# Optimization experiments

Measured on AMD Instinct MI355X. Metric: run time of the kernel, lower is better.

The kernel has to match this reference:

```python
import jax, jax.numpy as jnp
import numpy as np
from jax import lax

C = 128; G = 8; K = 3; P = K * K; GC = C // G
N, H, W = 4, 96, 96
EPS = 1e-5

def conv_bn_silu(x, w, gamma, beta, rmean, rvar, stride, pad):
    # Conv2d(bias=False) + BatchNorm2d(eval) + SiLU, NCHW
    y = lax.conv_general_dilated(x, w, (stride, stride), [(pad, pad), (pad, pad)],
                                 dimension_numbers=('NCHW', 'OIHW', 'NCHW'))
    s = gamma / jnp.sqrt(rvar + EPS)
    y = y * s[None, :, None, None] + (beta - rmean * s)[None, :, None, None]
    return y * jax.nn.sigmoid(y)

def dcnv3(x, dw_w, dw_b, ln_g, ln_b, off_w, off_b, m_w, m_b, ip_w, ip_b, op_w, op_b):
    # InternImage DCNv3, channels-last input (N,H,W,C), k=3 s=1 pad=1 dil=1 group=G, offset_scale=1
    n, h, w, c = x.shape
    xp = x @ ip_w.T + ip_b  # input_proj
    # offset/mask branch: depthwise 3x3 conv + LayerNorm + GELU on the ORIGINAL input
    dw = lax.conv_general_dilated(x, dw_w, (1, 1), [(1, 1), (1, 1)],
                                  dimension_numbers=('NHWC', 'HWIO', 'NHWC'),
                                  feature_group_count=c) + dw_b
    dw = (dw - dw.mean(-1, keepdims=True)) / jnp.sqrt(dw.var(-1, keepdims=True) + EPS) * ln_g + ln_b
    dw = jax.nn.gelu(dw)
    off = (dw @ off_w.T + off_b).reshape(n, h, w, G, P, 2)  # (..., (dx, dy))
    m = jax.nn.softmax((dw @ m_w.T + m_b).reshape(n, h, w, G, P), -1)
    pad = 1
    hp, wp = h + 2 * pad, w + 2 * pad
    xpad = jnp.pad(xp, ((0, 0), (pad, pad), (pad, pad), (0, 0))).reshape(n, hp, wp, G, GC)
    ky, kx = jnp.meshgrid(jnp.arange(-1, 2, dtype=x.dtype), jnp.arange(-1, 2, dtype=x.dtype), indexing='ij')
    # absolute sampling coords in padded image (grid_sample align_corners=False equivalent)
    py = (jnp.arange(h, dtype=x.dtype) + pad)[None, :, None, None, None] + ky.reshape(-1) + off[..., 1]
    px = (jnp.arange(w, dtype=x.dtype) + pad)[None, None, :, None, None] + kx.reshape(-1) + off[..., 0]
    yf = jnp.floor(py); xf = jnp.floor(px)
    wy = py - yf; wx = px - xf
    y0 = yf.astype(jnp.int32); x0 = xf.astype(jnp.int32)
    n_idx = jnp.arange(n)[:, None, None, None, None]
    g_idx = jnp.arange(G)[None, None, None, :, None]

    def gat(yi, xi):
        valid = ((yi >= 0) & (yi < hp) & (xi >= 0) & (xi < wp)).astype(x.dtype)
        v = xpad[n_idx, jnp.clip(yi, 0, hp - 1), jnp.clip(xi, 0, wp - 1), g_idx]  # (n,h,w,G,P,GC)
        return v * valid[..., None]

    v = (gat(y0, x0) * ((1 - wy) * (1 - wx))[..., None]
         + gat(y0, x0 + 1) * ((1 - wy) * wx)[..., None]
         + gat(y0 + 1, x0) * (wy * (1 - wx))[..., None]
         + gat(y0 + 1, x0 + 1) * (wy * wx)[..., None])
    out = jnp.einsum('nhwgpc,nhwgp->nhwgc', v, m).reshape(n, h, w, c)
    return out @ op_w.T + op_b  # output_proj

def _forward(x0, x1, x2, conv_w, conv_g, conv_b, conv_rm, conv_rv,
             conv1_w, conv1_g, conv1_b, conv1_rm, conv1_rv,
             conv2_w, conv2_g, conv2_b, conv2_rm, conv2_rv,
             dw_w, dw_b, ln_g, ln_b, off_w, off_b, m_w, m_b, ip_w, ip_b, op_w, op_b):
    n, _, h, w = x0.shape
    # x1: 256 ch > 128 -> self.conv (1x1); smaller spatial -> bilinear upsample to HW
    y1 = conv_bn_silu(x1, conv_w, conv_g, conv_b, conv_rm, conv_rv, 1, 0)
    feat_up1 = jax.image.resize(y1, (n, C, h, w), method='bilinear')
    # x2: 64 ch < 128 -> self.conv1 (1x1); larger spatial -> self.conv2 (3x3 s2) to HW
    y2 = conv_bn_silu(x2, conv1_w, conv1_g, conv1_b, conv1_rm, conv1_rv, 1, 0)
    feat_up2 = conv_bn_silu(y2, conv2_w, conv2_g, conv2_b, conv2_rm, conv2_rv, 2, 1)
    d1 = dcnv3(feat_up1.transpose(0, 2, 3, 1), dw_w, dw_b, ln_g, ln_b, off_w, off_b, m_w, m_b, ip_w, ip_b, op_w, op_b)
    d2 = dcnv3(feat_up2.transpose(0, 2, 3, 1), dw_w, dw_b, ln_g, ln_b, off_w, off_b, m_w, m_b, ip_w, ip_b, op_w, op_b)
    a1 = jax.nn.relu(d1).transpose(0, 3, 1, 2)
    a2 = jax.nn.relu(d2).transpose(0, 3, 1, 2)
    return jnp.concatenate([a1, x0, a2], axis=1)  # (N, 3C, H, W)

def setup_inputs():
    ks = jax.random.split(jax.random.key(0), 24)
    f = jnp.float32
    return {
        'x0': jax.random.normal(ks[0], (N, C, H, W), f),
        'x1': jax.random.normal(ks[1], (N, 2 * C, H // 2, W // 2), f),
        'x2': jax.random.normal(ks[2], (N, C // 2, 2 * H, 2 * W), f),
        'conv_w': jax.random.normal(ks[3], (C, 2 * C, 1, 1), f) * 0.05,
        'conv_g': jnp.ones((C,), f), 'conv_b': jnp.zeros((C,), f),
        'conv_rm': jax.random.normal(ks[4], (C,), f) * 0.1,
        'conv_rv': jax.random.uniform(ks[5], (C,), f) + 0.5,
        'conv1_w': jax.random.normal(ks[6], (C, C // 2, 1, 1), f) * 0.08,
        'conv1_g': jnp.ones((C,), f), 'conv1_b': jnp.zeros((C,), f),
        'conv1_rm': jax.random.normal(ks[7], (C,), f) * 0.1,
        'conv1_rv': jax.random.uniform(ks[8], (C,), f) + 0.5,
        'conv2_w': jax.random.normal(ks[9], (C, C, 3, 3), f) * 0.03,
        'conv2_g': jnp.ones((C,), f), 'conv2_b': jnp.zeros((C,), f),
        'conv2_rm': jax.random.normal(ks[10], (C,), f) * 0.1,
        'conv2_rv': jax.random.uniform(ks[11], (C,), f) + 0.5,
        'dw_w': jax.random.normal(ks[12], (3, 3, 1, C), f) * 0.1,
        'dw_b': jnp.zeros((C,), f),
        'ln_g': jnp.ones((C,), f), 'ln_b': jnp.zeros((C,), f),
        'off_w': jax.random.normal(ks[13], (G * P * 2, C), f) * 0.01,
        'off_b': jnp.zeros((G * P * 2,), f),
        'm_w': jax.random.normal(ks[14], (G * P, C), f) * 0.05,
        'm_b': jnp.zeros((G * P,), f),
        'ip_w': jax.random.normal(ks[15], (C, C), f) * 0.05,
        'ip_b': jnp.zeros((C,), f),
        'op_w': jax.random.normal(ks[16], (C, C), f) * 0.05,
        'op_b': jnp.zeros((C,), f),
    }

def reference(x0, x1, x2, conv_w, conv_g, conv_b, conv_rm, conv_rv,
              conv1_w, conv1_g, conv1_b, conv1_rm, conv1_rv,
              conv2_w, conv2_g, conv2_b, conv2_rm, conv2_rv,
              dw_w, dw_b, ln_g, ln_b, off_w, off_b, m_w, m_b, ip_w, ip_b, op_w, op_b):
    return _forward(x0, x1, x2, conv_w, conv_g, conv_b, conv_rm, conv_rv,
                    conv1_w, conv1_g, conv1_b, conv1_rm, conv1_rv,
                    conv2_w, conv2_g, conv2_b, conv2_rm, conv2_rv,
                    dw_w, dw_b, ln_g, ln_b, off_w, off_b, m_w, m_b, ip_w, ip_b, op_w, op_b)
```

## Files before the change

### kernel.cpp

```cpp
#include <hip/hip_runtime.h>
#include <cstdint>
#include <cstddef>

#define EPSV 1e-5f
#define NPIX 9216
#define LDA 136
#define LDK 72

typedef __bf16 bf16;
typedef _Float16 f16;
typedef __attribute__((ext_vector_type(8))) __bf16 bf16x8;
typedef __attribute__((ext_vector_type(4))) __bf16 bf16x4;
typedef __attribute__((ext_vector_type(2))) _Float16 f16x2;
typedef __attribute__((ext_vector_type(4))) float  f32x4;

__device__ __forceinline__ float silu_f(float v) { return v / (1.f + __expf(-v)); }

__global__ __launch_bounds__(256) void prep_kernel(
    const float* __restrict__ conv_w, const float* __restrict__ conv_g,
    const float* __restrict__ conv_b, const float* __restrict__ conv_rm, const float* __restrict__ conv_rv,
    const float* __restrict__ conv1_w, const float* __restrict__ conv1_g,
    const float* __restrict__ conv1_b, const float* __restrict__ conv1_rm, const float* __restrict__ conv1_rv,
    const float* __restrict__ conv2_w, const float* __restrict__ conv2_g,
    const float* __restrict__ conv2_bb, const float* __restrict__ conv2_rm, const float* __restrict__ conv2_rv,
    const float* __restrict__ ip_w, const float* __restrict__ op_w,
    const float* __restrict__ off_w, const float* __restrict__ m_w,
    const float* __restrict__ off_b, const float* __restrict__ m_b,
    float* __restrict__ WTSf, bf16* __restrict__ WTSb)
{
  int idx = blockIdx.x * 256 + threadIdx.x;
  if (idx < 608) {
    if (idx < 128) {
      int co = idx;
      float s = conv_g[co] * rsqrtf(conv_rv[co] + EPSV);
      WTSf[idx] = conv_b[co] - conv_rm[co] * s;
    } else if (idx < 256) {
      int co = idx - 128;
      float s = conv1_g[co] * rsqrtf(conv1_rv[co] + EPSV);
      WTSf[idx] = conv1_b[co] - conv1_rm[co] * s;
    } else if (idx < 384) {
      int co = idx - 256;
      float s = conv2_g[co] * rsqrtf(conv2_rv[co] + EPSV);
      WTSf[idx] = conv2_bb[co] - conv2_rm[co] * s;
    } else {
      int col = idx - 384;
      WTSf[idx] = (col < 144) ? off_b[col] : (col < 216 ? m_b[col - 144] : 0.f);
    }
  } else {
    int j = idx - 608;
    if (j < 32768) {
      int co = j >> 8, ci = j & 255;
      float s = conv_g[co] * rsqrtf(conv_rv[co] + EPSV);
      WTSb[j] = (bf16)(conv_w[co * 256 + ci] * s);
    } else if (j < 40960) {
      int r = j - 32768; int co = r >> 6, ci = r & 63;
      float s = conv1_g[co] * rsqrtf(conv1_rv[co] + EPSV);
      WTSb[j] = (bf16)(conv1_w[co * 64 + ci] * s);
    } else if (j < 188416) {
      int r = j - 40960; int kp = r >> 14; int rr = r & 16383;
      int co = rr >> 7, ci = rr & 127;
      float s = conv2_g[co] * rsqrtf(conv2_rv[co] + EPSV);
      WTSb[j] = (bf16)(conv2_w[(co * 128 + ci) * 9 + kp] * s);
    } else if (j < 204800) {
      int r = j - 188416; int co = r >> 7, ci = r & 127;
      WTSb[j] = (bf16)ip_w[co * 128 + ci];
    } else if (j < 233472) {
      int r = j - 204800; int co = r >> 7, ci = r & 127;
      float v = (co < 144) ? off_w[co * 128 + ci] : (co < 216 ? m_w[(co - 144) * 128 + ci] : 0.f);
      WTSb[j] = (bf16)v;
    } else if (j < 249856) {
      int r = j - 233472; int co = r >> 7, ci = r & 127;
      WTSb[j] = (bf16)op_w[co * 128 + ci];
    }
  }
}

__global__ __launch_bounds__(256) void c1x1_mfma_kernel(
    const float* __restrict__ x, const bf16* __restrict__ W,
    const float* __restrict__ bias, int K, int HW, bf16* __restrict__ outb)
{
  __shared__ bf16 As[64 * LDK];
  __shared__ bf16 Bs[128 * LDK];
  int m0 = blockIdx.x << 6;
  int t = threadIdx.x;
  int n = m0 / HW; int hw0 = m0 - n * HW;
  const float* xn = x + (size_t)n * K * HW;
  int wv = t >> 6, lane = t & 63;
  int lrow = lane & 15, q = lane >> 4;
  int n0 = wv * 32;
  f32x4 acc[4][2];
#pragma unroll
  for (int i = 0; i < 4; ++i)
#pragma unroll
    for (int j = 0; j < 2; ++j)
#pragma unroll
      for (int e = 0; e < 4; ++e) acc[i][j][e] = 0.f;

  for (int k0 = 0; k0 < K; k0 += 64) {
    if (k0) __syncthreads();
    for (int i = t; i < 1024; i += 256) {
      int px = i & 63; int ci4 = (i >> 6) << 2;
      bf16x4 p;
#pragma unroll
      for (int j = 0; j < 4; ++j)
        p[j] = (bf16)xn[(size_t)(k0 + ci4 + j) * HW + hw0 + px];
      *(bf16x4*)&As[px * LDK + ci4] = p;
    }
    for (int i = t; i < 1024; i += 256) {
      int co = i >> 3; int k8 = (i & 7) << 3;
      *(bf16x8*)&Bs[co * LDK + k8] = *(const bf16x8*)&W[(size_t)co * K + k0 + k8];
    }
    __syncthreads();
#pragma unroll
    for (int ks = 0; ks < 2; ++ks) {
      int ko = ks * 32 + q * 8;
      bf16x8 bfr0 = *(const bf16x8*)&Bs[(n0 + lrow) * LDK + ko];
      bf16x8 bfr1 = *(const bf16x8*)&Bs[(n0 + 16 + lrow) * LDK + ko];
#pragma unroll
      for (int mi = 0; mi < 4; ++mi) {
        bf16x8 afr = *(const bf16x8*)&As[(mi * 16 + lrow) * LDK + ko];
        acc[mi][0] = __builtin_amdgcn_mfma_f32_16x16x32_bf16(afr, bfr0, acc[mi][0], 0, 0, 0);
        acc[mi][1] = __builtin_amdgcn_mfma_f32_16x16x32_bf16(afr, bfr1, acc[mi][1], 0, 0, 0);
      }
    }
  }
#pragma unroll
  for (int mi = 0; mi < 4; ++mi) {
#pragma unroll
    for (int nj = 0; nj < 2; ++nj) {
      int co = n0 + nj * 16 + lrow;
      float bb = bias[co];
#pragma unroll
      for (int r = 0; r < 4; ++r) {
        int m = m0 + mi * 16 + q * 4 + r;
        outb[(size_t)m * 128 + co] = (bf16)silu_f(acc[mi][nj][r] + bb);
      }
    }
  }
}

__global__ __launch_bounds__(256) void upsample_kernel(
    const bf16* __restrict__ y1b, bf16* __restrict__ feat1b)
{
  int idx = blockIdx.x * 256 + threadIdx.x;
  int c4 = (idx & 31) << 2;
  int pw = idx >> 5;
  int ow = pw % 96; int t1 = pw / 96;
  int oh = t1 % 96; int n = t1 / 96;
  float sh = oh * 0.5f - 0.25f, sw = ow * 0.5f - 0.25f;
  float hf = floorf(sh), wf = floorf(sw);
  float fy = sh - hf, fx = sw - wf;
  int h0 = (int)hf, w0 = (int)wf;
  int h0c = max(h0, 0), h1c = min(h0 + 1, 47);
  int w0c = max(w0, 0), w1c = min(w0 + 1, 47);
  const bf16* yn = y1b + (size_t)n * 2304 * 128 + c4;
  bf16x4 v00 = *(const bf16x4*)&yn[(h0c * 48 + w0c) * 128];
  bf16x4 v01 = *(const bf16x4*)&yn[(h0c * 48 + w1c) * 128];
  bf16x4 v10 = *(const bf16x4*)&yn[(h1c * 48 + w0c) * 128];
  bf16x4 v11 = *(const bf16x4*)&yn[(h1c * 48 + w1c) * 128];
  bf16x4 o;
#pragma unroll
  for (int e = 0; e < 4; ++e) {
    float v = (1.f - fy) * ((1.f - fx) * (float)v00[e] + fx * (float)v01[e])
            + fy * ((1.f - fx) * (float)v10[e] + fx * (float)v11[e]);
    o[e] = (bf16)v;
  }
  *(bf16x4*)&feat1b[((size_t)n * NPIX + oh * 96 + ow) * 128 + c4] = o;
}

__global__ __launch_bounds__(256) void conv2_mfma_kernel(
    const bf16* __restrict__ y2b, const bf16* __restrict__ W2b,
    const float* __restrict__ b2, bf16* __restrict__ feat2b)
{
  __shared__ bf16 As[64 * LDA];
  __shared__ bf16 Bs[128 * LDA];
  int m0 = blockIdx.x << 6;
  int t = threadIdx.x;
  int wv = t >> 6, lane = t & 63;
  int lrow = lane & 15, q = lane >> 4;
  int n0 = wv * 32;
  f32x4 acc[4][2];
#pragma unroll
  for (int i = 0; i < 4; ++i)
#pragma unroll
    for (int j = 0; j < 2; ++j)
#pragma unroll
      for (int e = 0; e < 4; ++e) acc[i][j][e] = 0.f;
  bf16x8 zv;
#pragma unroll
  for (int e = 0; e < 8; ++e) zv[e] = (bf16)0.f;

  for (int kp = 0; kp < 9; ++kp) {
    int kh = kp / 3, kw = kp - kh * 3;
    __syncthreads();
    for (int i = t; i < 1024; i += 256) {
      int row = i >> 4; int c8 = (i & 15) << 3;
      int m = m0 + row;
      int nimg = m / NPIX; int hw = m - nimg * NPIX;
      int oh = hw / 96, ow = hw - oh * 96;
      int ih = 2 * oh - 1 + kh, iw = 2 * ow - 1 + kw;
      bf16x8 v = zv;
      if ((unsigned)ih < 192u && (unsigned)iw < 192u)
        v = *(const bf16x8*)&y2b[(((size_t)nimg * 192 + ih) * 192 + iw) * 128 + c8];
      *(bf16x8*)&As[row * LDA + c8] = v;
    }
    const bf16* Wk = W2b + kp * 16384;
    for (int i = t; i < 2048; i += 256) {
      int nn = i >> 4; int k8 = (i & 15) << 3;
      *(bf16x8*)&Bs[nn * LDA + k8] = *(const bf16x8*)&Wk[nn * 128 + k8];
    }
    __syncthreads();
#pragma unroll
    for (int ks = 0; ks < 4; ++ks) {
      bf16x8 bfr0 = *(const bf16x8*)&Bs[(n0 + lrow) * LDA + ks * 32 + q * 8];
      bf16x8 bfr1 = *(const bf16x8*)&Bs[(n0 + 16 + lrow) * LDA + ks * 32 + q * 8];
#pragma unroll
      for (int mi = 0; mi < 4; ++mi) {
        bf16x8 afr = *(const bf16x8*)&As[(mi * 16 + lrow) * LDA + ks * 32 + q * 8];
        acc[mi][0] = __builtin_amdgcn_mfma_f32_16x16x32_bf16(afr, bfr0, acc[mi][0], 0, 0, 0);
        acc[mi][1] = __builtin_amdgcn_mfma_f32_16x16x32_bf16(afr, bfr1, acc[mi][1], 0, 0, 0);
      }
    }
  }
#pragma unroll
  for (int mi = 0; mi < 4; ++mi) {
#pragma unroll
    for (int nj = 0; nj < 2; ++nj) {
      int co = n0 + nj * 16 + lrow;
      float bb = b2[co];
#pragma unroll
      for (int r = 0; r < 4; ++r) {
        int m = m0 + mi * 16 + q * 4 + r;
        feat2b[(size_t)m * 128 + co] = (bf16)silu_f(acc[mi][nj][r] + bb);
      }
    }
  }
}

__global__ __launch_bounds__(256) void mm_bf16_kernel(
    const bf16* __restrict__ A, const bf16* __restrict__ W,
    const float* __restrict__ bias, int Nc, int ostride, int act,
    int store_mode, void* __restrict__ outp)
{
  __shared__ bf16 As[64 * LDA];
  __shared__ bf16 Bs[128 * LDA];
  int m0 = blockIdx.x << 6;
  int nb = blockIdx.y << 7;
  int cols_here = Nc - nb; if (cols_here > 128) cols_here = 128;
  int t = threadIdx.x;
  for (int i = t; i < 1024; i += 256) {
    int row = i >> 4; int c8 = (i & 15) << 3;
    *(bf16x8*)&As[row * LDA + c8] = *(const bf16x8*)&A[(size_t)(m0 + row) * 128 + c8];
  }
  bf16x8 zv;
#pragma unroll
  for (int e = 0; e < 8; ++e) zv[e] = (bf16)0.f;
  for (int i = t; i < 2048; i += 256) {
    int n = i >> 4; int k8 = (i & 15) << 3;
    bf16x8 v = (n < cols_here) ? *(const bf16x8*)&W[(size_t)(nb + n) * 128 + k8] : zv;
    *(bf16x8*)&Bs[n * LDA + k8] = v;
  }
  __syncthreads();

  int wv = t >> 6, lane = t & 63;
  int lrow = lane & 15, q = lane >> 4;
  int n0 = wv * 32;
  f32x4 acc[4][2];
#pragma unroll
  for (int i = 0; i < 4; ++i)
#pragma unroll
    for (int j = 0; j < 2; ++j)
#pragma unroll
      for (int e = 0; e < 4; ++e) acc[i][j][e] = 0.f;

#pragma unroll
  for (int ks = 0; ks < 4; ++ks) {
    bf16x8 bfr0 = *(const bf16x8*)&Bs[(n0 + lrow) * LDA + ks * 32 + q * 8];
    bf16x8 bfr1 = *(const bf16x8*)&Bs[(n0 + 16 + lrow) * LDA + ks * 32 + q * 8];
#pragma unroll
    for (int mi = 0; mi < 4; ++mi) {
      bf16x8 afr = *(const bf16x8*)&As[(mi * 16 + lrow) * LDA + ks * 32 + q * 8];
      acc[mi][0] = __builtin_amdgcn_mfma_f32_16x16x32_bf16(afr, bfr0, acc[mi][0], 0, 0, 0);
      acc[mi][1] = __builtin_amdgcn_mfma_f32_16x16x32_bf16(afr, bfr1, acc[mi][1], 0, 0, 0);
    }
  }

  float* outf = (float*)outp;
  bf16*  outb = (bf16*)outp;
  f16*   outh = (f16*)outp;
#pragma unroll
  for (int mi = 0; mi < 4; ++mi) {
#pragma unroll
    for (int nj = 0; nj < 2; ++nj) {
      int col = nb + n0 + nj * 16 + lrow;
      if (col >= Nc) continue;
      float bb = bias[col];
#pragma unroll
      for (int r = 0; r < 4; ++r) {
        int m = m0 + mi * 16 + q * 4 + r;
        float v = acc[mi][nj][r] + bb;
        if (act == 1) v = fmaxf(v, 0.f);
        if (store_mode == 0) {
          outf[(size_t)m * ostride + col] = v;
        } else if (store_mode == 2) {
          outb[(size_t)m * 128 + col] = (bf16)v;
        } else if (store_mode == 3) {
          outh[(size_t)m * ostride + col] = (f16)v;
        } else {
          int nn = m / NPIX; int hw = m - nn * NPIX;
          int img = nn & 3; int choff = (nn >= 4) ? 256 : 0;
          outf[((size_t)(img * 384 + choff + col)) * NPIX + hw] = v;
        }
      }
    }
  }
}

__global__ __launch_bounds__(256) void dwom_kernel(
    const bf16* __restrict__ featb, const float* __restrict__ dw_w,
    const float* __restrict__ dw_b, const float* __restrict__ ln_g,
    const float* __restrict__ ln_b, const bf16* __restrict__ Wom,
    const float* __restrict__ bom, f16* __restrict__ offm)
{
  __shared__ float Wts[1152];
  __shared__ float Pb[384];
  __shared__ bf16 Ds[16 * LDA];
  int t = threadIdx.x;
  for (int i = t; i < 1152; i += 256) Wts[i] = dw_w[i];
  for (int i = t; i < 384; i += 256)
    Pb[i] = (i < 128) ? dw_b[i] : (i < 256 ? ln_g[i - 128] : ln_b[i - 256]);
  __syncthreads();

  int bid = blockIdx.x;
  int wg = (bid & 7) * 576 + (bid >> 3);
  {
    int pxl = t >> 4;
    int c8 = (t & 15) << 3;
    int pixel = wg * 16 + pxl;
    int n = pixel / NPIX; int hw = pixel - n * NPIX;
    int h = hw / 96; int w = hw - h * 96;
    const bf16* fn = featb + (size_t)n * NPIX * 128 + c8;
    bf16x8 zv;
#pragma unroll
    for (int e = 0; e < 8; ++e) zv[e] = (bf16)0.f;

    bf16x8 v[9];
#pragma unroll
    for (int p = 0; p < 9; ++p) {
      int hh = h + p / 3 - 1, ww = w + (p % 3) - 1;
      bool valid = ((unsigned)hh < 96u) && ((unsigned)ww < 96u);
      int hc = min(max(hh, 0), 95), wc = min(max(ww, 0), 95);
      bf16x8 x = *(const bf16x8*)&fn[(hc * 96 + wc) * 128];
      v[p] = valid ? x : zv;
    }

    float acc[8];
#pragma unroll
    for (int e = 0; e < 8; ++e) acc[e] = Pb[c8 + e];
#pragma unroll
    for (int p = 0; p < 9; ++p) {
      f32x4 w0 = *(const f32x4*)&Wts[p * 128 + c8];
      f32x4 w1 = *(const f32x4*)&Wts[p * 128 + c8 + 4];
#pragma unroll
      for (int e = 0; e < 4; ++e) {
        acc[e]     += (float)v[p][e]     * w0[e];
        acc[4 + e] += (float)v[p][4 + e] * w1[e];
      }
    }

    float s = 0.f, qs = 0.f;
#pragma unroll
    for (int e = 0; e < 8; ++e) { s += acc[e]; qs += acc[e] * acc[e]; }
#pragma unroll
    for (int off = 8; off > 0; off >>= 1) {
      s  += __shfl_xor(s, off);
      qs += __shfl_xor(qs, off);
    }
    float mean = s * (1.f / 128.f);
    float var = qs * (1.f / 128.f) - mean * mean;
    float rstd = rsqrtf(var + EPSV);
    bf16x8 o;
#pragma unroll
    for (int e = 0; e < 8; ++e) {
      float xn = (acc[e] - mean) * rstd * Pb[128 + c8 + e] + Pb[256 + c8 + e];
      float z = 0.7978845608028654f * (xn + 0.044715f * xn * xn * xn);
      float th;
      if (z > 15.f) th = 1.f;
      else if (z < -15.f) th = -1.f;
      else { float e2 = __expf(2.f * z); th = (e2 - 1.f) / (e2 + 1.f); }
      o[e] = (bf16)(0.5f * xn * (1.f + th));
    }
    *(bf16x8*)&Ds[pxl * LDA + c8] = o;
  }
  __syncthreads();

  {
    int wv = t >> 6, lane = t & 63;
    int lrow = lane & 15, q = lane >> 4;
    f16* orow = offm + (size_t)(wg * 16) * 224;
    for (int gsel = wv; gsel < 7; gsel += 4) {
      int n0 = gsel * 32;
      f32x4 pacc[2];
#pragma unroll
      for (int j = 0; j < 2; ++j)
#pragma unroll
        for (int e = 0; e < 4; ++e) pacc[j][e] = 0.f;
#pragma unroll
      for (int ks = 0; ks < 4; ++ks) {
        int ko = ks * 32 + q * 8;
        bf16x8 afr  = *(const bf16x8*)&Ds[lrow * LDA + ko];
        bf16x8 bfr0 = *(const bf16x8*)&Wom[(size_t)(n0 + lrow) * 128 + ko];
        bf16x8 bfr1 = *(const bf16x8*)&Wom[(size_t)(n0 + 16 + lrow) * 128 + ko];
        pacc[0] = __builtin_amdgcn_mfma_f32_16x16x32_bf16(afr, bfr0, pacc[0], 0, 0, 0);
        pacc[1] = __builtin_amdgcn_mfma_f32_16x16x32_bf16(afr, bfr1, pacc[1], 0, 0, 0);
      }
#pragma unroll
      for (int nj = 0; nj < 2; ++nj) {
        int col = n0 + nj * 16 + lrow;
        float bb = bom[col];
#pragma unroll
        for (int r = 0; r < 4; ++r) {
          int px = q * 4 + r;
          orow[(size_t)px * 224 + col] = (f16)(pacc[nj][r] + bb);
        }
      }
    }
  }
}

__global__ __launch_bounds__(512, 6) void sample_kernel(
    const bf16* __restrict__ xpb, const f16* __restrict__ offm,
    const bf16* __restrict__ Wop, const float* __restrict__ op_b,
    float* __restrict__ out)
{
  __shared__ char LB[32256];
  uint32_t* Sd = (uint32_t*)LB;
  float*    Pm = (float*)(LB + 14336);
  bf16*     Avs = (bf16*)(LB + 23552);
  float*    Cs = (float*)LB;
  const f16* S = (const f16*)Sd;
  int t = threadIdx.x;
  int bid = blockIdx.x;
  int wg = (bid & 7) * 288 + (bid >> 3);
  {
    const uint32_t* src = (const uint32_t*)(offm + (size_t)wg * 32 * 224);
    for (int i = t; i < 3584; i += 512) Sd[i] = src[i];
  }
  __syncthreads();
  if (t < 256) {
    int px = t >> 3, gg = t & 7;
    const f16* L = S + px * 224 + 144 + gg * 9;
    float l[9]; float mx = -1e30f;
#pragma unroll
    for (int p = 0; p < 9; ++p) { l[p] = (float)L[p]; mx = fmaxf(mx, l[p]); }
    float se = 0.f;
#pragma unroll
    for (int p = 0; p < 9; ++p) { l[p] = __expf(l[p] - mx); se += l[p]; }
    float inv = 1.f / se;
    float* Pp = Pm + px * 72 + gg * 9;
#pragma unroll
    for (int p = 0; p < 9; ++p) Pp[p] = l[p] * inv;
  }
  __syncthreads();
  {
    int pxl = t >> 4;
    int tid16 = t & 15;
    int g = tid16 >> 1;
    int c8 = (tid16 & 1) << 3;
    int pixel = wg * 32 + pxl;
    int n = pixel / NPIX; int hw = pixel - n * NPIX;
    int h = hw / 96; int w = hw - h * 96;
    const f16* Sp = S + pxl * 224 + g * 18;
    const float* Pp = Pm + pxl * 72 + g * 9;
    const bf16* xpn = xpb + (size_t)n * NPIX * 128 + g * 16 + c8;
    float acc[8];
#pragma unroll
    for (int e = 0; e < 8; ++e) acc[e] = 0.f;
#pragma unroll 1
    for (int kh = 0; kh < 3; ++kh) {
#pragma unroll
      for (int kw = 0; kw < 3; ++kw) {
        int p = kh * 3 + kw;
        f16x2 d2 = *(const f16x2*)&Sp[p * 2];
        float dx = (float)d2.x, dy = (float)d2.y;
        float pyu = (float)(h + kh - 1) + dy;
        float pxu = (float)(w + kw - 1) + dx;
        float yf = floorf(pyu), xf = floorf(pxu);
        float wy = pyu - yf, wx = pxu - xf;
        int y0 = (int)yf, x0 = (int)xf;
        float ay0 = ((unsigned)y0 < 96u) ? (1.f - wy) : 0.f;
        float ay1 = ((unsigned)(y0 + 1) < 96u) ? wy : 0.f;
        float ax0 = ((unsigned)x0 < 96u) ? (1.f - wx) : 0.f;
        float ax1 = ((unsigned)(x0 + 1) < 96u) ? wx : 0.f;
        int y0c = min(max(y0, 0), 95), y1c = min(max(y0 + 1, 0), 95);
        int x0c = min(max(x0, 0), 95), x1c = min(max(x0 + 1, 0), 95);
        float mp = Pp[p];
        float w00 = ay0 * ax0 * mp, w01 = ay0 * ax1 * mp;
        float w10 = ay1 * ax0 * mp, w11 = ay1 * ax1 * mp;
        bf16x8 v00 = *(const bf16x8*)&xpn[(y0c * 96 + x0c) * 128];
        bf16x8 v01 = *(const bf16x8*)&xpn[(y0c * 96 + x1c) * 128];
        bf16x8 v10 = *(const bf16x8*)&xpn[(y1c * 96 + x0c) * 128];
        bf16x8 v11 = *(const bf16x8*)&xpn[(y1c * 96 + x1c) * 128];
#pragma unroll
        for (int e = 0; e < 8; ++e) {
          acc[e] += w00 * (float)v00[e] + w01 * (float)v01[e]
                  + w10 * (float)v10[e] + w11 * (float)v11[e];
        }
      }
    }
    bf16x8 o;
#pragma unroll
    for (int e = 0; e < 8; ++e) o[e] = (bf16)acc[e];
    *(bf16x8*)&Avs[pxl * LDA + g * 16 + c8] = o;
  }
  __syncthreads();

  {
    int wv = t >> 6, lane = t & 63;
    int lrow = lane & 15, q = lane >> 4;
    int mrow0 = (wv & 1) * 16;
    int n0 = (wv >> 1) * 32;
    f32x4 pacc[2];
#pragma unroll
    for (int j = 0; j < 2; ++j)
#pragma unroll
      for (int e = 0; e < 4; ++e) pacc[j][e] = 0.f;
#pragma unroll
    for (int ks = 0; ks < 4; ++ks) {
      int ko = ks * 32 + q * 8;
      bf16x8 afr  = *(const bf16x8*)&Avs[(mrow0 + lrow) * LDA + ko];
      bf16x8 bfr0 = *(const bf16x8*)&Wop[(size_t)(n0 + lrow) * 128 + ko];
      bf16x8 bfr1 = *(const bf16x8*)&Wop[(size_t)(n0 + 16 + lrow) * 128 + ko];
      pacc[0] = __builtin_amdgcn_mfma_f32_16x16x32_bf16(afr, bfr0, pacc[0], 0, 0, 0);
      pacc[1] = __builtin_amdgcn_mfma_f32_16x16x32_bf16(afr, bfr1, pacc[1], 0, 0, 0);
    }
#pragma unroll
    for (int nj = 0; nj < 2; ++nj) {
      int col = n0 + nj * 16 + lrow;
      float bb = op_b[col];
#pragma unroll
      for (int r = 0; r < 4; ++r) {
        int px = mrow0 + q * 4 + r;
        Cs[col * 33 + px] = fmaxf(pacc[nj][r] + bb, 0.f);
      }
    }
  }
  __syncthreads();

  {
    int nn = (wg * 32) / NPIX;
    int hwb = wg * 32 - nn * NPIX;
    int img = nn & 3; int choff = (nn >= 4) ? 256 : 0;
    float* ob = out + (size_t)(img * 384 + choff) * NPIX + hwb;
#pragma unroll
    for (int i = t; i < 1024; i += 512) {
      int col = i >> 3, f4 = i & 7;
      f32x4 v = *(const f32x4*)&Cs[col * 33 + f4 * 4];
      *(f32x4*)&ob[(size_t)col * NPIX + f4 * 4] = v;
    }
  }
}

__global__ __launch_bounds__(256) void copy_x0_kernel(
    const float4* __restrict__ x0, float4* __restrict__ out)
{
  int idx = blockIdx.x * 256 + threadIdx.x;
  int n = idx / (128 * 2304);
  int r = idx - n * (128 * 2304);
  out[(size_t)(n * 384 + 128) * 2304 + r] = x0[(size_t)n * 128 * 2304 + r];
}

extern "C" void kernel_launch(void* const* d_in, const int* in_sizes, int n_in,
                              void* d_out, int out_size, void* d_ws, size_t ws_size,
                              hipStream_t stream)
{
  (void)in_sizes; (void)n_in; (void)out_size; (void)ws_size;
  const float* x0      = (const float*)d_in[0];
  const float* x1      = (const float*)d_in[1];
  const float* x2      = (const float*)d_in[2];
  const float* conv_w  = (const float*)d_in[3];
  const float* conv_g  = (const float*)d_in[4];
  const float* conv_b  = (const float*)d_in[5];
  const float* conv_rm = (const float*)d_in[6];
  const float* conv_rv = (const float*)d_in[7];
  const float* conv1_w = (const float*)d_in[8];
  const float* conv1_g = (const float*)d_in[9];
  const float* conv1_b = (const float*)d_in[10];
  const float* conv1_rm= (const float*)d_in[11];
  const float* conv1_rv= (const float*)d_in[12];
  const float* conv2_w = (const float*)d_in[13];
  const float* conv2_g = (const float*)d_in[14];
  const float* conv2_b = (const float*)d_in[15];
  const float* conv2_rm= (const float*)d_in[16];
  const float* conv2_rv= (const float*)d_in[17];
  const float* dw_w    = (const float*)d_in[18];
  const float* dw_b    = (const float*)d_in[19];
  const float* ln_g    = (const float*)d_in[20];
  const float* ln_b    = (const float*)d_in[21];
  const float* off_w   = (const float*)d_in[22];
  const float* off_b   = (const float*)d_in[23];
  const float* m_w     = (const float*)d_in[24];
  const float* m_b     = (const float*)d_in[25];
  const float* ip_w    = (const float*)d_in[26];
  const float* ip_b    = (const float*)d_in[27];
  const float* op_w    = (const float*)d_in[28];
  const float* op_b    = (const float*)d_in[29];
  float* out = (float*)d_out;
  char* WS = (char*)d_ws;

  bf16* featb  = (bf16*)WS;
  bf16* feat1b = featb;
  bf16* feat2b = featb + 4718592;
  bf16* y2b    = (bf16*)(WS + 18874368);
  bf16* xpb    = (bf16*)(WS + 18874368);
  bf16* y1b    = (bf16*)(WS + 56623104);
  f16*  offm   = (f16*)(WS + 58982400);
  float* WTSf  = (float*)(WS + 125042688);
  bf16*  WTSb  = (bf16*)(WS + 125045120);

  float* b1f  = WTSf;
  float* b1bf = WTSf + 128;
  float* b2f  = WTSf + 256;
  float* bomf = WTSf + 384;
  bf16* W1b  = WTSb;
  bf16* W1bb = WTSb + 32768;
  bf16* W2b  = WTSb + 40960;
  bf16* Wipb = WTSb + 188416;
  bf16* Womb = WTSb + 204800;
  bf16* Wopb = WTSb + 233472;

  prep_kernel<<<979, 256, 0, stream>>>(
      conv_w, conv_g, conv_b, conv_rm, conv_rv,
      conv1_w, conv1_g, conv1_b, conv1_rm, conv1_rv,
      conv2_w, conv2_g, conv2_b, conv2_rm, conv2_rv,
      ip_w, op_w, off_w, m_w, off_b, m_b, WTSf, WTSb);

  c1x1_mfma_kernel<<<144, 256, 0, stream>>>(x1, W1b, b1f, 256, 2304, y1b);
  upsample_kernel<<<4608, 256, 0, stream>>>(y1b, feat1b);

  c1x1_mfma_kernel<<<2304, 256, 0, stream>>>(x2, W1bb, b1bf, 64, 36864, y2b);
  conv2_mfma_kernel<<<576, 256, 0, stream>>>(y2b, W2b, b2f, feat2b);

  mm_bf16_kernel<<<dim3(1152, 1), 256, 0, stream>>>(featb, Wipb, ip_b, 128, 128, 0, 2, xpb);
  dwom_kernel<<<4608, 256, 0, stream>>>(featb, dw_w, dw_b, ln_g, ln_b, Womb, bomf, offm);
  sample_kernel<<<2304, 512, 0, stream>>>(xpb, offm, Wopb, op_b, out);

  copy_x0_kernel<<<4608, 256, 0, stream>>>((const float4*)x0, (float4*)out);
}
```

Baseline: 371.8 us.

## Fuse input_proj GEMM into upsample and conv2 epilogues

Removes the standalone input_proj GEMM over all 73728 pixels. The projection now runs inside the upsample kernel, on 16-pixel tiles staged in shared memory, and inside the conv2 kernel's epilogue, where the post-SiLU tile is reused from LDS. Both kernels write feat and xp with coalesced vector stores. This saves one launch and one full read of the feature buffer. In exchange, weight fragments are read straight from global memory in every block, the upsample kernel now uses small 16-row MFMA tiles, and xpb moves to a separate workspace region so it no longer aliases y2b.

```diff
diff --git a/kernel.cpp b/kernel.cpp
--- a/kernel.cpp
+++ b/kernel.cpp
@@ -139,38 +139,84 @@
   }
 }
 
-__global__ __launch_bounds__(256) void upsample_kernel(
-    const bf16* __restrict__ y1b, bf16* __restrict__ feat1b)
-{
-  int idx = blockIdx.x * 256 + threadIdx.x;
-  int c4 = (idx & 31) << 2;
-  int pw = idx >> 5;
-  int ow = pw % 96; int t1 = pw / 96;
-  int oh = t1 % 96; int n = t1 / 96;
-  float sh = oh * 0.5f - 0.25f, sw = ow * 0.5f - 0.25f;
-  float hf = floorf(sh), wf = floorf(sw);
-  float fy = sh - hf, fx = sw - wf;
-  int h0 = (int)hf, w0 = (int)wf;
-  int h0c = max(h0, 0), h1c = min(h0 + 1, 47);
-  int w0c = max(w0, 0), w1c = min(w0 + 1, 47);
-  const bf16* yn = y1b + (size_t)n * 2304 * 128 + c4;
-  bf16x4 v00 = *(const bf16x4*)&yn[(h0c * 48 + w0c) * 128];
-  bf16x4 v01 = *(const bf16x4*)&yn[(h0c * 48 + w1c) * 128];
-  bf16x4 v10 = *(const bf16x4*)&yn[(h1c * 48 + w0c) * 128];
-  bf16x4 v11 = *(const bf16x4*)&yn[(h1c * 48 + w1c) * 128];
-  bf16x4 o;
-#pragma unroll
-  for (int e = 0; e < 4; ++e) {
-    float v = (1.f - fy) * ((1.f - fx) * (float)v00[e] + fx * (float)v01[e])
-            + fy * ((1.f - fx) * (float)v10[e] + fx * (float)v11[e]);
-    o[e] = (bf16)v;
-  }
-  *(bf16x4*)&feat1b[((size_t)n * NPIX + oh * 96 + ow) * 128 + c4] = o;
+__global__ __launch_bounds__(256) void upsample_ip_kernel(
+    const bf16* __restrict__ y1b, const bf16* __restrict__ Wip,
+    const float* __restrict__ ip_b, bf16* __restrict__ feat1b,
+    bf16* __restrict__ xpb)
+{
+  __shared__ bf16 Ds[16 * LDA];
+  __shared__ bf16 Xs[16 * LDA];
+  int t = threadIdx.x;
+  int wg = blockIdx.x;
+  int pixel0 = wg * 16;
+  {
+    int pxl = t >> 4;
+    int c8 = (t & 15) << 3;
+    int pixel = pixel0 + pxl;
+    int n = pixel / NPIX; int hw = pixel - n * NPIX;
+    int oh = hw / 96; int ow = hw - oh * 96;
+    float sh = oh * 0.5f - 0.25f, sw = ow * 0.5f - 0.25f;
+    float hf = floorf(sh), wf = floorf(sw);
+    float fy = sh - hf, fx = sw - wf;
+    int h0 = (int)hf, w0 = (int)wf;
+    int h0c = max(h0, 0), h1c = min(h0 + 1, 47);
+    int w0c = max(w0, 0), w1c = min(w0 + 1, 47);
+    const bf16* yn = y1b + (size_t)n * 2304 * 128 + c8;
+    bf16x8 v00 = *(const bf16x8*)&yn[(h0c * 48 + w0c) * 128];
+    bf16x8 v01 = *(const bf16x8*)&yn[(h0c * 48 + w1c) * 128];
+    bf16x8 v10 = *(const bf16x8*)&yn[(h1c * 48 + w0c) * 128];
+    bf16x8 v11 = *(const bf16x8*)&yn[(h1c * 48 + w1c) * 128];
+    bf16x8 o;
+#pragma unroll
+    for (int e = 0; e < 8; ++e) {
+      float v = (1.f - fy) * ((1.f - fx) * (float)v00[e] + fx * (float)v01[e])
+              + fy * ((1.f - fx) * (float)v10[e] + fx * (float)v11[e]);
+      o[e] = (bf16)v;
+    }
+    *(bf16x8*)&feat1b[(size_t)pixel * 128 + c8] = o;
+    *(bf16x8*)&Ds[pxl * LDA + c8] = o;
+  }
+  __syncthreads();
+  {
+    int wv = t >> 6, lane = t & 63;
+    int lrow = lane & 15, q = lane >> 4;
+    int n0 = wv * 32;
+    f32x4 pacc[2];
+#pragma unroll
+    for (int j = 0; j < 2; ++j)
+#pragma unroll
+      for (int e = 0; e < 4; ++e) pacc[j][e] = 0.f;
+#pragma unroll
+    for (int ks = 0; ks < 4; ++ks) {
+      int ko = ks * 32 + q * 8;
+      bf16x8 afr  = *(const bf16x8*)&Ds[lrow * LDA + ko];
+      bf16x8 bfr0 = *(const bf16x8*)&Wip[(size_t)(n0 + lrow) * 128 + ko];
+      bf16x8 bfr1 = *(const bf16x8*)&Wip[(size_t)(n0 + 16 + lrow) * 128 + ko];
+      pacc[0] = __builtin_amdgcn_mfma_f32_16x16x32_bf16(afr, bfr0, pacc[0], 0, 0, 0);
+      pacc[1] = __builtin_amdgcn_mfma_f32_16x16x32_bf16(afr, bfr1, pacc[1], 0, 0, 0);
+    }
+#pragma unroll
+    for (int nj = 0; nj < 2; ++nj) {
+      int col = n0 + nj * 16 + lrow;
+      float bb = ip_b[col];
+#pragma unroll
+      for (int r = 0; r < 4; ++r)
+        Xs[(q * 4 + r) * LDA + col] = (bf16)(pacc[nj][r] + bb);
+    }
+  }
+  __syncthreads();
+  {
+    int pxl = t >> 4;
+    int c8 = (t & 15) << 3;
+    *(bf16x8*)&xpb[(size_t)(pixel0 + pxl) * 128 + c8] = *(const bf16x8*)&Xs[pxl * LDA + c8];
+  }
 }
 
 __global__ __launch_bounds__(256) void conv2_mfma_kernel(
     const bf16* __restrict__ y2b, const bf16* __restrict__ W2b,
-    const float* __restrict__ b2, bf16* __restrict__ feat2b)
+    const float* __restrict__ b2, const bf16* __restrict__ Wip,
+    const float* __restrict__ ip_b, bf16* __restrict__ feat2b,
+    bf16* __restrict__ xpb)
 {
   __shared__ bf16 As[64 * LDA];
   __shared__ bf16 Bs[128 * LDA];
@@ -222,6 +268,8 @@
       }
     }
   }
+  __syncthreads();
+  bf16* Fs = Bs;
 #pragma unroll
   for (int mi = 0; mi < 4; ++mi) {
 #pragma unroll
@@ -230,89 +278,46 @@
       float bb = b2[co];
 #pragma unroll
       for (int r = 0; r < 4; ++r) {
-        int m = m0 + mi * 16 + q * 4 + r;
-        feat2b[(size_t)m * 128 + co] = (bf16)silu_f(acc[mi][nj][r] + bb);
-      }
-    }
-  }
-}
-
-__global__ __launch_bounds__(256) void mm_bf16_kernel(
-    const bf16* __restrict__ A, const bf16* __restrict__ W,
-    const float* __restrict__ bias, int Nc, int ostride, int act,
-    int store_mode, void* __restrict__ outp)
-{
-  __shared__ bf16 As[64 * LDA];
-  __shared__ bf16 Bs[128 * LDA];
-  int m0 = blockIdx.x << 6;
-  int nb = blockIdx.y << 7;
-  int cols_here = Nc - nb; if (cols_here > 128) cols_here = 128;
-  int t = threadIdx.x;
+        int row = mi * 16 + q * 4 + r;
+        Fs[row * LDA + co] = (bf16)silu_f(acc[mi][nj][r] + bb);
+      }
+    }
+  }
+  __syncthreads();
+  bf16* Xs = As;
+  {
+    int mrow0 = wv * 16;
+    for (int g = 0; g < 4; ++g) {
+      int ng = g * 32;
+      f32x4 pacc[2];
+#pragma unroll
+      for (int j = 0; j < 2; ++j)
+#pragma unroll
+        for (int e = 0; e < 4; ++e) pacc[j][e] = 0.f;
+#pragma unroll
+      for (int ks = 0; ks < 4; ++ks) {
+        int ko = ks * 32 + q * 8;
+        bf16x8 afr  = *(const bf16x8*)&Fs[(mrow0 + lrow) * LDA + ko];
+        bf16x8 bfr0 = *(const bf16x8*)&Wip[(size_t)(ng + lrow) * 128 + ko];
+        bf16x8 bfr1 = *(const bf16x8*)&Wip[(size_t)(ng + 16 + lrow) * 128 + ko];
+        pacc[0] = __builtin_amdgcn_mfma_f32_16x16x32_bf16(afr, bfr0, pacc[0], 0, 0, 0);
+        pacc[1] = __builtin_amdgcn_mfma_f32_16x16x32_bf16(afr, bfr1, pacc[1], 0, 0, 0);
+      }
+#pragma unroll
+      for (int nj = 0; nj < 2; ++nj) {
+        int col = ng + nj * 16 + lrow;
+        float bb = ip_b[col];
+#pragma unroll
+        for (int r = 0; r < 4; ++r)
+          Xs[(mrow0 + q * 4 + r) * LDA + col] = (bf16)(pacc[nj][r] + bb);
+      }
+    }
+  }
+  __syncthreads();
   for (int i = t; i < 1024; i += 256) {
     int row = i >> 4; int c8 = (i & 15) << 3;
-    *(bf16x8*)&As[row * LDA + c8] = *(const bf16x8*)&A[(size_t)(m0 + row) * 128 + c8];
-  }
-  bf16x8 zv;
-#pragma unroll
-  for (int e = 0; e < 8; ++e) zv[e] = (bf16)0.f;
-  for (int i = t; i < 2048; i += 256) {
-    int n = i >> 4; int k8 = (i & 15) << 3;
-    bf16x8 v = (n < cols_here) ? *(const bf16x8*)&W[(size_t)(nb + n) * 128 + k8] : zv;
-    *(bf16x8*)&Bs[n * LDA + k8] = v;
-  }
-  __syncthreads();
-
-  int wv = t >> 6, lane = t & 63;
-  int lrow = lane & 15, q = lane >> 4;
-  int n0 = wv * 32;
-  f32x4 acc[4][2];
-#pragma unroll
-  for (int i = 0; i < 4; ++i)
-#pragma unroll
-    for (int j = 0; j < 2; ++j)
-#pragma unroll
-      for (int e = 0; e < 4; ++e) acc[i][j][e] = 0.f;
-
-#pragma unroll
-  for (int ks = 0; ks < 4; ++ks) {
-    bf16x8 bfr0 = *(const bf16x8*)&Bs[(n0 + lrow) * LDA + ks * 32 + q * 8];
-    bf16x8 bfr1 = *(const bf16x8*)&Bs[(n0 + 16 + lrow) * LDA + ks * 32 + q * 8];
-#pragma unroll
-    for (int mi = 0; mi < 4; ++mi) {
-      bf16x8 afr = *(const bf16x8*)&As[(mi * 16 + lrow) * LDA + ks * 32 + q * 8];
-      acc[mi][0] = __builtin_amdgcn_mfma_f32_16x16x32_bf16(afr, bfr0, acc[mi][0], 0, 0, 0);
-      acc[mi][1] = __builtin_amdgcn_mfma_f32_16x16x32_bf16(afr, bfr1, acc[mi][1], 0, 0, 0);
-    }
-  }
-
-  float* outf = (float*)outp;
-  bf16*  outb = (bf16*)outp;
-  f16*   outh = (f16*)outp;
-#pragma unroll
-  for (int mi = 0; mi < 4; ++mi) {
-#pragma unroll
-    for (int nj = 0; nj < 2; ++nj) {
-      int col = nb + n0 + nj * 16 + lrow;
-      if (col >= Nc) continue;
-      float bb = bias[col];
-#pragma unroll
-      for (int r = 0; r < 4; ++r) {
-        int m = m0 + mi * 16 + q * 4 + r;
-        float v = acc[mi][nj][r] + bb;
-        if (act == 1) v = fmaxf(v, 0.f);
-        if (store_mode == 0) {
-          outf[(size_t)m * ostride + col] = v;
-        } else if (store_mode == 2) {
-          outb[(size_t)m * 128 + col] = (bf16)v;
-        } else if (store_mode == 3) {
-          outh[(size_t)m * ostride + col] = (f16)v;
-        } else {
-          int nn = m / NPIX; int hw = m - nn * NPIX;
-          int img = nn & 3; int choff = (nn >= 4) ? 256 : 0;
-          outf[((size_t)(img * 384 + choff + col)) * NPIX + hw] = v;
-        }
-      }
-    }
+    *(bf16x8*)&feat2b[(size_t)(m0 + row) * 128 + c8] = *(const bf16x8*)&Fs[row * LDA + c8];
+    *(bf16x8*)&xpb[(size_t)(36864 + m0 + row) * 128 + c8] = *(const bf16x8*)&Xs[row * LDA + c8];
   }
 }
 
@@ -612,9 +617,9 @@
   bf16* feat1b = featb;
   bf16* feat2b = featb + 4718592;
   bf16* y2b    = (bf16*)(WS + 18874368);
-  bf16* xpb    = (bf16*)(WS + 18874368);
   bf16* y1b    = (bf16*)(WS + 56623104);
   f16*  offm   = (f16*)(WS + 58982400);
+  bf16* xpb    = (bf16*)(WS + 92012544);
   float* WTSf  = (float*)(WS + 125042688);
   bf16*  WTSb  = (bf16*)(WS + 125045120);
 
@@ -636,12 +641,11 @@
       ip_w, op_w, off_w, m_w, off_b, m_b, WTSf, WTSb);
 
   c1x1_mfma_kernel<<<144, 256, 0, stream>>>(x1, W1b, b1f, 256, 2304, y1b);
-  upsample_kernel<<<4608, 256, 0, stream>>>(y1b, feat1b);
+  upsample_ip_kernel<<<2304, 256, 0, stream>>>(y1b, Wipb, ip_b, feat1b, xpb);
 
   c1x1_mfma_kernel<<<2304, 256, 0, stream>>>(x2, W1bb, b1bf, 64, 36864, y2b);
-  conv2_mfma_kernel<<<576, 256, 0, stream>>>(y2b, W2b, b2f, feat2b);
-
-  mm_bf16_kernel<<<dim3(1152, 1), 256, 0, stream>>>(featb, Wipb, ip_b, 128, 128, 0, 2, xpb);
+  conv2_mfma_kernel<<<576, 256, 0, stream>>>(y2b, W2b, b2f, Wipb, ip_b, feat2b, xpb);
+
   dwom_kernel<<<4608, 256, 0, stream>>>(featb, dw_w, dw_b, ln_g, ln_b, Womb, bomf, offm);
   sample_kernel<<<2304, 512, 0, stream>>>(xpb, offm, Wopb, op_b, out);
 
```

After: 377.1 us. About the same (+1.4%).

## Merge 1x1 convs, specialize ip matmul, fold x0 copy into sampler launch

Applied to the files above, without the earlier changes.

Merges the two 1x1 conv launches into one grid that dispatches on block index, so both branches can run together. The generic matmul is specialized into a fixed 128-column bf16-output kernel, which drops the runtime store-mode and bounds branches. The x0 passthrough copy moves into extra blocks of the sampling kernel, removing a separate launch. The cost is that copy blocks now launch with 512 threads and the sampler's shared-memory footprint, which may affect how they are scheduled.

```diff
diff --git a/kernel.cpp b/kernel.cpp
--- a/kernel.cpp
+++ b/kernel.cpp
@@ -75,13 +75,10 @@
   }
 }
 
-__global__ __launch_bounds__(256) void c1x1_mfma_kernel(
-    const float* __restrict__ x, const bf16* __restrict__ W,
-    const float* __restrict__ bias, int K, int HW, bf16* __restrict__ outb)
-{
-  __shared__ bf16 As[64 * LDK];
-  __shared__ bf16 Bs[128 * LDK];
-  int m0 = blockIdx.x << 6;
+__device__ __forceinline__ void c1x1_body(
+    bf16* As, bf16* Bs, const float* __restrict__ x, const bf16* __restrict__ W,
+    const float* __restrict__ bias, int K, int HW, int m0, bf16* __restrict__ outb)
+{
   int t = threadIdx.x;
   int n = m0 / HW; int hw0 = m0 - n * HW;
   const float* xn = x + (size_t)n * K * HW;
@@ -136,6 +133,21 @@
         outb[(size_t)m * 128 + co] = (bf16)silu_f(acc[mi][nj][r] + bb);
       }
     }
+  }
+}
+
+__global__ __launch_bounds__(256) void c1x1_dual_kernel(
+    const float* __restrict__ x1, const bf16* __restrict__ W1b, const float* __restrict__ b1f,
+    const float* __restrict__ x2, const bf16* __restrict__ W1bb, const float* __restrict__ b1bf,
+    bf16* __restrict__ y1b, bf16* __restrict__ y2b)
+{
+  __shared__ bf16 As[64 * LDK];
+  __shared__ bf16 Bs[128 * LDK];
+  int bid = blockIdx.x;
+  if (bid < 2304) {
+    c1x1_body(As, Bs, x2, W1bb, b1bf, 64, 36864, bid << 6, y2b);
+  } else {
+    c1x1_body(As, Bs, x1, W1b, b1f, 256, 2304, (bid - 2304) << 6, y1b);
   }
 }
 
@@ -237,28 +249,21 @@
   }
 }
 
-__global__ __launch_bounds__(256) void mm_bf16_kernel(
+__global__ __launch_bounds__(256) void mm_ip_kernel(
     const bf16* __restrict__ A, const bf16* __restrict__ W,
-    const float* __restrict__ bias, int Nc, int ostride, int act,
-    int store_mode, void* __restrict__ outp)
+    const float* __restrict__ bias, bf16* __restrict__ outb)
 {
   __shared__ bf16 As[64 * LDA];
   __shared__ bf16 Bs[128 * LDA];
   int m0 = blockIdx.x << 6;
-  int nb = blockIdx.y << 7;
-  int cols_here = Nc - nb; if (cols_here > 128) cols_here = 128;
   int t = threadIdx.x;
   for (int i = t; i < 1024; i += 256) {
     int row = i >> 4; int c8 = (i & 15) << 3;
     *(bf16x8*)&As[row * LDA + c8] = *(const bf16x8*)&A[(size_t)(m0 + row) * 128 + c8];
   }
-  bf16x8 zv;
-#pragma unroll
-  for (int e = 0; e < 8; ++e) zv[e] = (bf16)0.f;
   for (int i = t; i < 2048; i += 256) {
     int n = i >> 4; int k8 = (i & 15) << 3;
-    bf16x8 v = (n < cols_here) ? *(const bf16x8*)&W[(size_t)(nb + n) * 128 + k8] : zv;
-    *(bf16x8*)&Bs[n * LDA + k8] = v;
+    *(bf16x8*)&Bs[n * LDA + k8] = *(const bf16x8*)&W[(size_t)n * 128 + k8];
   }
   __syncthreads();
 
@@ -284,33 +289,16 @@
       acc[mi][1] = __builtin_amdgcn_mfma_f32_16x16x32_bf16(afr, bfr1, acc[mi][1], 0, 0, 0);
     }
   }
-
-  float* outf = (float*)outp;
-  bf16*  outb = (bf16*)outp;
-  f16*   outh = (f16*)outp;
 #pragma unroll
   for (int mi = 0; mi < 4; ++mi) {
 #pragma unroll
     for (int nj = 0; nj < 2; ++nj) {
-      int col = nb + n0 + nj * 16 + lrow;
-      if (col >= Nc) continue;
+      int col = n0 + nj * 16 + lrow;
       float bb = bias[col];
 #pragma unroll
       for (int r = 0; r < 4; ++r) {
         int m = m0 + mi * 16 + q * 4 + r;
-        float v = acc[mi][nj][r] + bb;
-        if (act == 1) v = fmaxf(v, 0.f);
-        if (store_mode == 0) {
-          outf[(size_t)m * ostride + col] = v;
-        } else if (store_mode == 2) {
-          outb[(size_t)m * 128 + col] = (bf16)v;
-        } else if (store_mode == 3) {
-          outh[(size_t)m * ostride + col] = (f16)v;
-        } else {
-          int nn = m / NPIX; int hw = m - nn * NPIX;
-          int img = nn & 3; int choff = (nn >= 4) ? 256 : 0;
-          outf[((size_t)(img * 384 + choff + col)) * NPIX + hw] = v;
-        }
+        outb[(size_t)m * 128 + col] = (bf16)(acc[mi][nj][r] + bb);
       }
     }
   }
@@ -428,19 +416,27 @@
   }
 }
 
-__global__ __launch_bounds__(512, 6) void sample_kernel(
+__global__ __launch_bounds__(512, 6) void sample_copy_kernel(
     const bf16* __restrict__ xpb, const f16* __restrict__ offm,
     const bf16* __restrict__ Wop, const float* __restrict__ op_b,
-    float* __restrict__ out)
+    const float4* __restrict__ x0, float* __restrict__ out)
 {
   __shared__ char LB[32256];
+  int t = threadIdx.x;
+  int bid = blockIdx.x;
+  if (bid >= 2304) {
+    int idx = (bid - 2304) * 512 + t;
+    int n = idx / (128 * 2304);
+    int r = idx - n * (128 * 2304);
+    float4* outv = (float4*)out;
+    outv[(size_t)(n * 384 + 128) * 2304 + r] = x0[(size_t)n * 128 * 2304 + r];
+    return;
+  }
   uint32_t* Sd = (uint32_t*)LB;
   float*    Pm = (float*)(LB + 14336);
   bf16*     Avs = (bf16*)(LB + 23552);
   float*    Cs = (float*)LB;
   const f16* S = (const f16*)Sd;
-  int t = threadIdx.x;
-  int bid = blockIdx.x;
   int wg = (bid & 7) * 288 + (bid >> 3);
   {
     const uint32_t* src = (const uint32_t*)(offm + (size_t)wg * 32 * 224);
@@ -487,13 +483,13 @@
         float pxu = (float)(w + kw - 1) + dx;
         float yf = floorf(pyu), xf = floorf(pxu);
         float wy = pyu - yf, wx = pxu - xf;
-        int y0 = (int)yf, x0 = (int)xf;
+        int y0 = (int)yf, x0i = (int)xf;
         float ay0 = ((unsigned)y0 < 96u) ? (1.f - wy) : 0.f;
         float ay1 = ((unsigned)(y0 + 1) < 96u) ? wy : 0.f;
-        float ax0 = ((unsigned)x0 < 96u) ? (1.f - wx) : 0.f;
-        float ax1 = ((unsigned)(x0 + 1) < 96u) ? wx : 0.f;
+        float ax0 = ((unsigned)x0i < 96u) ? (1.f - wx) : 0.f;
+        float ax1 = ((unsigned)(x0i + 1) < 96u) ? wx : 0.f;
         int y0c = min(max(y0, 0), 95), y1c = min(max(y0 + 1, 0), 95);
-        int x0c = min(max(x0, 0), 95), x1c = min(max(x0 + 1, 0), 95);
+        int x0c = min(max(x0i, 0), 95), x1c = min(max(x0i + 1, 0), 95);
         float mp = Pp[p];
         float w00 = ay0 * ax0 * mp, w01 = ay0 * ax1 * mp;
         float w10 = ay1 * ax0 * mp, w11 = ay1 * ax1 * mp;
@@ -559,15 +555,6 @@
       *(f32x4*)&ob[(size_t)col * NPIX + f4 * 4] = v;
     }
   }
-}
-
-__global__ __launch_bounds__(256) void copy_x0_kernel(
-    const float4* __restrict__ x0, float4* __restrict__ out)
-{
-  int idx = blockIdx.x * 256 + threadIdx.x;
-  int n = idx / (128 * 2304);
-  int r = idx - n * (128 * 2304);
-  out[(size_t)(n * 384 + 128) * 2304 + r] = x0[(size_t)n * 128 * 2304 + r];
 }
 
 extern "C" void kernel_launch(void* const* d_in, const int* in_sizes, int n_in,
@@ -635,15 +622,14 @@
       conv2_w, conv2_g, conv2_b, conv2_rm, conv2_rv,
       ip_w, op_w, off_w, m_w, off_b, m_b, WTSf, WTSb);
 
-  c1x1_mfma_kernel<<<144, 256, 0, stream>>>(x1, W1b, b1f, 256, 2304, y1b);
+  c1x1_dual_kernel<<<2448, 256, 0, stream>>>(x1, W1b, b1f, x2, W1bb, b1bf, y1b, y2b);
+
   upsample_kernel<<<4608, 256, 0, stream>>>(y1b, feat1b);
-
-  c1x1_mfma_kernel<<<2304, 256, 0, stream>>>(x2, W1bb, b1bf, 64, 36864, y2b);
   conv2_mfma_kernel<<<576, 256, 0, stream>>>(y2b, W2b, b2f, feat2b);
 
-  mm_bf16_kernel<<<dim3(1152, 1), 256, 0, stream>>>(featb, Wipb, ip_b, 128, 128, 0, 2, xpb);
+  mm_ip_kernel<<<1152, 256, 0, stream>>>(featb, Wipb, ip_b, xpb);
   dwom_kernel<<<4608, 256, 0, stream>>>(featb, dw_w, dw_b, ln_g, ln_b, Womb, bomf, offm);
-  sample_kernel<<<2304, 512, 0, stream>>>(xpb, offm, Wopb, op_b, out);
-
-  copy_x0_kernel<<<4608, 256, 0, stream>>>((const float4*)x0, (float4*)out);
-}
+
+  sample_copy_kernel<<<4608, 512, 0, stream>>>(xpb, offm, Wopb, op_b,
+                                               (const float4*)x0, out);
+}
```

After: 355.5 us. -4.4%, faster.
